# Performance work log

Hardware: AMD Instinct MI355X
Metric: run time of the kernel (lower is better)

## Reference

```python
import jax, jax.numpy as jnp
import numpy as np

WEIGHTS = (0.5, 1.0, 2.0)   # per-channel weights (init kwarg)
INVERTED = True             # init kwarg


def setup_inputs() -> dict:
    key = jax.random.key(0)
    B, C, H, W = 16, 3, 256, 256
    # binary flood mask: nonzero = foreground (scipy EDT measures distance to nearest zero)
    flood = jax.random.randint(key, (B, C, H, W), 0, 2).astype(jnp.float32)
    return {"flood_batch": flood}


def _edt_squared(mask):
    """Exact squared Euclidean distance transform per [H,W] slice.

    mask: bool [B,C,H,W], True = foreground (nonzero). Returns float32 [B,C,H,W]
    squared distance from each True pixel to the nearest False pixel (0 at False).
    Uses the exact separable decomposition:
      D2[r,w] = min_{r'} ( g[r',w]^2 + (r-r')^2 ),  g = 1D horizontal distance to zero.
    """
    B, C, H, W = mask.shape
    BIG = jnp.float32(H + W)  # exceeds any achievable 1D distance

    # --- pass 1: 1D distance to nearest zero along W (forward + backward scans) ---
    m = jnp.moveaxis(mask, -1, 0)  # [W,B,C,H]

    def step(carry, mm):
        d = jnp.where(mm, jnp.minimum(carry + 1.0, BIG), 0.0)
        return d, d

    init = jnp.full((B, C, H), BIG, jnp.float32)
    _, fwd = jax.lax.scan(step, init, m)
    _, bwd = jax.lax.scan(step, init, m[::-1])
    g = jnp.minimum(fwd, bwd[::-1])          # [W,B,C,H]
    g2 = jnp.moveaxis(g, 0, -1) ** 2          # [B,C,H,W]

    # --- pass 2: exact min-plus over rows (vectorized over B,C,W; scan over output row) ---
    rows = jnp.arange(H, dtype=jnp.float32)

    def row_step(_, r):
        cand = g2 + ((r - rows) ** 2)[None, None, :, None]  # [B,C,H,W]
        return None, cand.min(axis=2)                        # [B,C,W]

    _, d2 = jax.lax.scan(row_step, None, rows)  # [H,B,C,W]
    return jnp.moveaxis(d2, 0, 2)               # [B,C,H,W]


def reference(flood_batch):
    w = jnp.asarray(WEIGHTS, jnp.float32)
    dt = jnp.sqrt(_edt_squared(flood_batch != 0))            # [B,C,H,W]
    dt = dt * w[None, :, None, None]                         # per-channel weight
    mx = dt.max(axis=(2, 3), keepdims=True)                  # per-slice max
    safe = jnp.where(mx > 0, mx, 1.0)
    scaled = (mx - dt) / safe if INVERTED else dt / safe
    return jnp.where(mx > 0, scaled, dt)
```

## Files before the change

kernel.cpp:

```cpp
#include <hip/hip_runtime.h>


#define PADV 1e30f

__global__ __launch_bounds__(256) void k1_bitmask(const float* __restrict__ in,
                                                  unsigned long long* __restrict__ bits) {
    int row = blockIdx.x * 4 + (threadIdx.x >> 6);
    int lane = threadIdx.x & 63;
    const float4 m = ((const float4*)in)[(long)row * 64 + lane];

    unsigned long long b0 = __ballot(m.x == 0.f);
    unsigned long long b1 = __ballot(m.y == 0.f);
    unsigned long long b2 = __ballot(m.z == 0.f);
    unsigned long long b3 = __ballot(m.w == 0.f);
    if (lane == 0) {
        ulonglong4* dst = (ulonglong4*)(bits + (long)row * 4);
        ulonglong4 v; v.x = b0; v.y = b1; v.z = b2; v.w = b3;
        *dst = v;
    }
}

__global__ __launch_bounds__(256) __attribute__((amdgpu_waves_per_eu(4)))
void k2_colpass(const unsigned long long* __restrict__ bits,
                float* __restrict__ d2out,
                float* __restrict__ stripmax) {
    __shared__ __align__(16) float tile[16 * 289];
    __shared__ float wm[4];
    unsigned long long* bm = (unsigned long long*)tile;

    int bx = blockIdx.x;
    int slice = bx >> 4;
    int w0 = (bx & 15) * 16;
    int tid = threadIdx.x;

    {
        const unsigned long long* src = bits + (long)slice * 1024;
        #pragma unroll
        for (int i = 0; i < 4; ++i) bm[i * 256 + tid] = src[i * 256 + tid];
    }
    __syncthreads();

    int c = tid & 15;
    int p = w0 + c;
    int rg = tid >> 4;
    int r0 = rg * 16;

    unsigned long long mLo[4], mHi[4];
    int qv[4];
    #pragma unroll
    for (int cc = 0; cc < 4; ++cc) {
        int q = p - cc;
        int qa = (q < 0) ? 0 : q;
        int tp = qa >> 2;
        mLo[cc] = (q >= 0) ? (~0ull >> (63 - tp)) : 0ull;
        int tn = (q < 0) ? 0 : ((q + 3) >> 2);
        mHi[cc] = (tn < 64) ? (~0ull << tn) : 0ull;
        qv[cc] = q;
    }

    const ulonglong2* bmv = (const ulonglong2*)bm;
    float own[16];
    #pragma unroll
    for (int k = 0; k < 16; ++k) {
        int kk = (k + rg) & 15;
        int r = r0 + kk;
        ulonglong2 wa = bmv[r * 2];
        ulonglong2 wb = bmv[r * 2 + 1];
        unsigned long long M[4] = { wa.x, wa.y, wb.x, wb.y };
        int dist = 512;
        #pragma unroll
        for (int cc = 0; cc < 4; ++cc) {
            unsigned long long Ml = M[cc] & mLo[cc];
            unsigned long long Mh = M[cc] & mHi[cc];
            if (Ml) dist = min(dist, qv[cc] - 4 * (63 - __builtin_clzll(Ml)));
            if (Mh) dist = min(dist, 4 * __builtin_ctzll(Mh) - qv[cc]);
        }
        float fd = (float)dist;
        own[kk] = fd * fd;
    }
    __syncthreads();

    {
        int cc = tid >> 4, i = tid & 15;
        tile[cc * 289 + i] = PADV;
        tile[cc * 289 + 272 + i] = PADV;
    }
    #pragma unroll
    for (int k = 0; k < 16; ++k)
        tile[c * 289 + 16 + r0 + k] = own[k];
    __syncthreads();

    float lo[16], hi[16];
    #pragma unroll
    for (int i = 0; i < 16; ++i) {
        lo[i] = tile[c * 289 + r0 + i];
        hi[i] = tile[c * 289 + 32 + r0 + i];
    }

    float dmin[16];
    #pragma unroll
    for (int k = 0; k < 16; ++k) dmin[k] = own[k];
    #pragma unroll
    for (int o = 1; o <= 16; ++o) {
        float oo = (float)(o * o);
        #pragma unroll
        for (int k = 0; k < 16; ++k) {
            int jm = k - o, jp = k + o;
            float a = (jm >= 0) ? own[jm] : lo[jm + 16];
            float b = (jp < 16) ? own[jp] : hi[jp - 16];
            dmin[k] = fminf(dmin[k], fminf(a, b) + oo);
        }
    }

    #pragma unroll
    for (int k = 0; k < 16; ++k) {
        if (dmin[k] > 288.0f) {
            float best = dmin[k];
            int r = r0 + k;
            for (int rp = 0; rp < 256; ++rp) {
                float dr = (float)(r - rp);
                best = fminf(best, fmaf(dr, dr, tile[c * 289 + 16 + rp]));
            }
            dmin[k] = best;
        }
    }

    float* dst = d2out + (long)slice * 65536 + w0 + c;
    float m = 0.f;
    #pragma unroll
    for (int k = 0; k < 16; ++k) {
        dst[(long)(r0 + k) * 256] = dmin[k];
        m = fmaxf(m, dmin[k]);
    }
    #pragma unroll
    for (int off = 32; off >= 1; off >>= 1)
        m = fmaxf(m, __shfl_down(m, off, 64));
    if ((tid & 63) == 0) wm[tid >> 6] = m;
    __syncthreads();
    if (tid == 0)
        stripmax[bx] = fmaxf(fmaxf(wm[0], wm[1]), fmaxf(wm[2], wm[3]));
}

__global__ __launch_bounds__(256) void k3_final(float* __restrict__ out,
                                                const float* __restrict__ stripmax) {
    __shared__ float sMx;
    int tid = threadIdx.x;
    int idx4 = blockIdx.x * 256 + tid;
    int slice = blockIdx.x >> 6;
    if (tid < 16) {
        float v = stripmax[slice * 16 + tid];
        #pragma unroll
        for (int off = 8; off >= 1; off >>= 1) v = fmaxf(v, __shfl_down(v, off, 64));
        if (tid == 0) sMx = v;
    }
    __syncthreads();

    int c = slice % 3;
    float wgt = (c == 0) ? 0.5f : ((c == 1) ? 1.0f : 2.0f);
    float mx = wgt * __builtin_sqrtf(sMx);

    float4 d2 = ((float4*)out)[idx4];
    float4 r;
    if (mx > 0.f) {
        float inv = 1.0f / mx;
        r.x = (mx - wgt * __builtin_sqrtf(d2.x)) * inv;
        r.y = (mx - wgt * __builtin_sqrtf(d2.y)) * inv;
        r.z = (mx - wgt * __builtin_sqrtf(d2.z)) * inv;
        r.w = (mx - wgt * __builtin_sqrtf(d2.w)) * inv;
    } else {
        r.x = wgt * __builtin_sqrtf(d2.x);
        r.y = wgt * __builtin_sqrtf(d2.y);
        r.z = wgt * __builtin_sqrtf(d2.z);
        r.w = wgt * __builtin_sqrtf(d2.w);
    }
    ((float4*)out)[idx4] = r;
}

extern "C" void kernel_launch(void* const* d_in, const int* in_sizes, int n_in,
                              void* d_out, int out_size, void* d_ws, size_t ws_size,
                              hipStream_t stream) {
    const float* in = (const float*)d_in[0];
    float* out = (float*)d_out;
    float* stripmax = (float*)d_ws;
    unsigned long long* bits = (unsigned long long*)((char*)d_ws + 4096);

    k1_bitmask<<<3072, 256, 0, stream>>>(in, bits);
    k2_colpass<<<768, 256, 0, stream>>>(bits, out, stripmax);
    k3_final<<<3072, 256, 0, stream>>>(out, stripmax);
}
```

Measured before the change: 86.59 us.

## Compute horizontal distances in bitmask kernel, store uint16, split column pass into halves

The row-wise 1D distance-to-zero is now computed in the first kernel from the wave ballot masks and written as a 16-bit array, instead of storing bitmasks and recomputing distances in the column kernel. The column kernel now loads only a 160-row window of the 16-bit distances per block and handles half a slice column strip, doubling the grid to 1536 blocks with 8 rows per thread. The rare far-distance fallback reads the full column from global memory instead of shared memory. This trades a larger intermediate buffer (2 bytes per pixel vs 1 bit) for more parallelism and less per-thread work and register use.

```diff
diff --git a/kernel.cpp b/kernel.cpp
--- a/kernel.cpp
+++ b/kernel.cpp
@@ -3,139 +3,162 @@
 
 #define PADV 1e30f
 
-__global__ __launch_bounds__(256) void k1_bitmask(const float* __restrict__ in,
-                                                  unsigned long long* __restrict__ bits) {
+__global__ __launch_bounds__(256) void k1_g16(const float* __restrict__ in,
+                                              unsigned short* __restrict__ g) {
     int row = blockIdx.x * 4 + (threadIdx.x >> 6);
     int lane = threadIdx.x & 63;
     const float4 m = ((const float4*)in)[(long)row * 64 + lane];
 
-    unsigned long long b0 = __ballot(m.x == 0.f);
-    unsigned long long b1 = __ballot(m.y == 0.f);
-    unsigned long long b2 = __ballot(m.z == 0.f);
-    unsigned long long b3 = __ballot(m.w == 0.f);
-    if (lane == 0) {
-        ulonglong4* dst = (ulonglong4*)(bits + (long)row * 4);
-        ulonglong4 v; v.x = b0; v.y = b1; v.z = b2; v.w = b3;
-        *dst = v;
-    }
+    unsigned long long b[4];
+    b[0] = __ballot(m.x == 0.f);
+    b[1] = __ballot(m.y == 0.f);
+    b[2] = __ballot(m.z == 0.f);
+    b[3] = __ballot(m.w == 0.f);
+
+    unsigned long long loP = ~0ull >> (63 - lane);
+    unsigned long long loM = loP >> 1;
+    unsigned long long hiP = ~0ull << lane;
+    unsigned long long hiM = hiP << 1;
+
+    int LP[4], LM[4], RP[4], RM[4];
+    #pragma unroll
+    for (int cc = 0; cc < 4; ++cc) {
+        unsigned long long mlp = b[cc] & loP;
+        unsigned long long mlm = b[cc] & loM;
+        unsigned long long mhp = b[cc] & hiP;
+        unsigned long long mhm = b[cc] & hiM;
+        LP[cc] = mlp ? 4 * (63 - __builtin_clzll(mlp)) + cc : -1000;
+        LM[cc] = mlm ? 4 * (63 - __builtin_clzll(mlm)) + cc : -1000;
+        RP[cc] = mhp ? 4 * __builtin_ctzll(mhp) + cc : 2000;
+        RM[cc] = mhm ? 4 * __builtin_ctzll(mhm) + cc : 2000;
+    }
+    int qp1 = max(LP[0], LP[1]);
+    int qp2 = max(qp1, LP[2]);
+    int qp3 = max(qp2, LP[3]);
+    int sm3 = LM[3];
+    int sm2 = max(LM[2], sm3);
+    int sm1 = max(LM[1], sm2);
+    int colL0 = max(LP[0], sm1);
+    int colL1 = max(qp1, sm2);
+    int colL2 = max(qp2, sm3);
+    int colL3 = qp3;
+    int sp2 = min(RP[2], RP[3]);
+    int sp1 = min(RP[1], sp2);
+    int sp0 = min(RP[0], sp1);
+    int pm0 = RM[0];
+    int pm1 = min(pm0, RM[1]);
+    int pm2 = min(pm1, RM[2]);
+    int colR0 = sp0;
+    int colR1 = min(pm0, sp1);
+    int colR2 = min(pm1, sp2);
+    int colR3 = min(pm2, RP[3]);
+
+    int p0 = lane * 4;
+    int d0 = min(min(p0 - colL0, colR0 - p0), 512);
+    int d1 = min(min(p0 + 1 - colL1, colR1 - p0 - 1), 512);
+    int d2 = min(min(p0 + 2 - colL2, colR2 - p0 - 2), 512);
+    int d3 = min(min(p0 + 3 - colL3, colR3 - p0 - 3), 512);
+
+    ushort4 v;
+    v.x = (unsigned short)d0; v.y = (unsigned short)d1;
+    v.z = (unsigned short)d2; v.w = (unsigned short)d3;
+    ((ushort4*)(g + (long)row * 256))[lane] = v;
 }
 
 __global__ __launch_bounds__(256) __attribute__((amdgpu_waves_per_eu(4)))
-void k2_colpass(const unsigned long long* __restrict__ bits,
+void k2_colpass(const unsigned short* __restrict__ g,
                 float* __restrict__ d2out,
                 float* __restrict__ stripmax) {
-    __shared__ __align__(16) float tile[16 * 289];
+    __shared__ float tile[16 * 161];
     __shared__ float wm[4];
-    unsigned long long* bm = (unsigned long long*)tile;
-
     int bx = blockIdx.x;
-    int slice = bx >> 4;
-    int w0 = (bx & 15) * 16;
+    int slice = bx >> 5;
+    int sub = bx & 31;
+    int strip = sub >> 1;
+    int half = sub & 1;
+    int w0 = strip * 16;
+    int base = half * 128;
     int tid = threadIdx.x;
 
-    {
-        const unsigned long long* src = bits + (long)slice * 1024;
-        #pragma unroll
-        for (int i = 0; i < 4; ++i) bm[i * 256 + tid] = src[i * 256 + tid];
+    if (tid < 160) {
+        int r = base - 16 + tid;
+        if (r >= 0 && r < 256) {
+            const uint4* src = (const uint4*)(g + (long)slice * 65536 + (long)r * 256 + w0);
+            #pragma unroll
+            for (int j = 0; j < 2; ++j) {
+                uint4 q = src[j];
+                unsigned vv[4] = {q.x, q.y, q.z, q.w};
+                #pragma unroll
+                for (int e = 0; e < 4; ++e) {
+                    float dl = (float)(vv[e] & 0xffffu);
+                    float dh = (float)(vv[e] >> 16);
+                    int col = j * 8 + e * 2;
+                    tile[col * 161 + tid] = dl * dl;
+                    tile[(col + 1) * 161 + tid] = dh * dh;
+                }
+            }
+        } else {
+            #pragma unroll
+            for (int cc = 0; cc < 16; ++cc) tile[cc * 161 + tid] = PADV;
+        }
     }
     __syncthreads();
 
     int c = tid & 15;
-    int p = w0 + c;
     int rg = tid >> 4;
-    int r0 = rg * 16;
-
-    unsigned long long mLo[4], mHi[4];
-    int qv[4];
-    #pragma unroll
-    for (int cc = 0; cc < 4; ++cc) {
-        int q = p - cc;
-        int qa = (q < 0) ? 0 : q;
-        int tp = qa >> 2;
-        mLo[cc] = (q >= 0) ? (~0ull >> (63 - tp)) : 0ull;
-        int tn = (q < 0) ? 0 : ((q + 3) >> 2);
-        mHi[cc] = (tn < 64) ? (~0ull << tn) : 0ull;
-        qv[cc] = q;
-    }
-
-    const ulonglong2* bmv = (const ulonglong2*)bm;
-    float own[16];
-    #pragma unroll
-    for (int k = 0; k < 16; ++k) {
-        int kk = (k + rg) & 15;
-        int r = r0 + kk;
-        ulonglong2 wa = bmv[r * 2];
-        ulonglong2 wb = bmv[r * 2 + 1];
-        unsigned long long M[4] = { wa.x, wa.y, wb.x, wb.y };
-        int dist = 512;
-        #pragma unroll
-        for (int cc = 0; cc < 4; ++cc) {
-            unsigned long long Ml = M[cc] & mLo[cc];
-            unsigned long long Mh = M[cc] & mHi[cc];
-            if (Ml) dist = min(dist, qv[cc] - 4 * (63 - __builtin_clzll(Ml)));
-            if (Mh) dist = min(dist, 4 * __builtin_ctzll(Mh) - qv[cc]);
-        }
-        float fd = (float)dist;
-        own[kk] = fd * fd;
-    }
-    __syncthreads();
-
-    {
-        int cc = tid >> 4, i = tid & 15;
-        tile[cc * 289 + i] = PADV;
-        tile[cc * 289 + 272 + i] = PADV;
-    }
-    #pragma unroll
-    for (int k = 0; k < 16; ++k)
-        tile[c * 289 + 16 + r0 + k] = own[k];
-    __syncthreads();
-
-    float lo[16], hi[16];
+    int i0 = 16 + rg * 8;
+    float own[8], lo[16], hi[16];
+    #pragma unroll
+    for (int k = 0; k < 8; ++k) own[k] = tile[c * 161 + i0 + k];
     #pragma unroll
     for (int i = 0; i < 16; ++i) {
-        lo[i] = tile[c * 289 + r0 + i];
-        hi[i] = tile[c * 289 + 32 + r0 + i];
-    }
-
-    float dmin[16];
-    #pragma unroll
-    for (int k = 0; k < 16; ++k) dmin[k] = own[k];
+        lo[i] = tile[c * 161 + i0 - 16 + i];
+        hi[i] = tile[c * 161 + i0 + 8 + i];
+    }
+
+    float dmin[8];
+    #pragma unroll
+    for (int k = 0; k < 8; ++k) dmin[k] = own[k];
     #pragma unroll
     for (int o = 1; o <= 16; ++o) {
         float oo = (float)(o * o);
         #pragma unroll
-        for (int k = 0; k < 16; ++k) {
+        for (int k = 0; k < 8; ++k) {
             int jm = k - o, jp = k + o;
             float a = (jm >= 0) ? own[jm] : lo[jm + 16];
-            float b = (jp < 16) ? own[jp] : hi[jp - 16];
+            float b = (jp < 8) ? own[jp] : hi[jp - 8];
             dmin[k] = fminf(dmin[k], fminf(a, b) + oo);
         }
     }
 
-    #pragma unroll
-    for (int k = 0; k < 16; ++k) {
+    int p = w0 + c;
+    int r0 = base + rg * 8;
+    #pragma unroll
+    for (int k = 0; k < 8; ++k) {
         if (dmin[k] > 288.0f) {
             float best = dmin[k];
             int r = r0 + k;
+            const unsigned short* col = g + (long)slice * 65536 + p;
             for (int rp = 0; rp < 256; ++rp) {
+                float gv = (float)col[rp * 256];
                 float dr = (float)(r - rp);
-                best = fminf(best, fmaf(dr, dr, tile[c * 289 + 16 + rp]));
+                best = fminf(best, fmaf(dr, dr, gv * gv));
             }
             dmin[k] = best;
         }
     }
 
     float* dst = d2out + (long)slice * 65536 + w0 + c;
-    float m = 0.f;
-    #pragma unroll
-    for (int k = 0; k < 16; ++k) {
+    float mmax = 0.f;
+    #pragma unroll
+    for (int k = 0; k < 8; ++k) {
         dst[(long)(r0 + k) * 256] = dmin[k];
-        m = fmaxf(m, dmin[k]);
+        mmax = fmaxf(mmax, dmin[k]);
     }
     #pragma unroll
     for (int off = 32; off >= 1; off >>= 1)
-        m = fmaxf(m, __shfl_down(m, off, 64));
-    if ((tid & 63) == 0) wm[tid >> 6] = m;
+        mmax = fmaxf(mmax, __shfl_down(mmax, off, 64));
+    if ((tid & 63) == 0) wm[tid >> 6] = mmax;
     __syncthreads();
     if (tid == 0)
         stripmax[bx] = fmaxf(fmaxf(wm[0], wm[1]), fmaxf(wm[2], wm[3]));
@@ -147,10 +170,10 @@
     int tid = threadIdx.x;
     int idx4 = blockIdx.x * 256 + tid;
     int slice = blockIdx.x >> 6;
-    if (tid < 16) {
-        float v = stripmax[slice * 16 + tid];
+    if (tid < 32) {
+        float v = stripmax[slice * 32 + tid];
         #pragma unroll
-        for (int off = 8; off >= 1; off >>= 1) v = fmaxf(v, __shfl_down(v, off, 64));
+        for (int off = 16; off >= 1; off >>= 1) v = fmaxf(v, __shfl_down(v, off, 64));
         if (tid == 0) sMx = v;
     }
     __syncthreads();
@@ -182,9 +205,9 @@
     const float* in = (const float*)d_in[0];
     float* out = (float*)d_out;
     float* stripmax = (float*)d_ws;
-    unsigned long long* bits = (unsigned long long*)((char*)d_ws + 4096);
-
-    k1_bitmask<<<3072, 256, 0, stream>>>(in, bits);
-    k2_colpass<<<768, 256, 0, stream>>>(bits, out, stripmax);
+    unsigned short* g = (unsigned short*)((char*)d_ws + 8192);
+
+    k1_g16<<<3072, 256, 0, stream>>>(in, g);
+    k2_colpass<<<1536, 256, 0, stream>>>(g, out, stripmax);
     k3_final<<<3072, 256, 0, stream>>>(out, stripmax);
 }
```

Result: faster. 80.30 us, median of 2 (-7.3%).
